# Performance work log

Hardware: AMD Instinct MI355X
Metric: run time of the kernel (lower is better)

Reference implementation:

```python
import jax, jax.numpy as jnp
import numpy as np

S, R = 512, 384            # N_seq, N_res
C_MSA, C_Z = 64, 128
C_HID, H = 32, 8
INF = 1e8
EPS = 1e-5


def _layernorm(x, w, b):
    mu = jnp.mean(x, axis=-1, keepdims=True)
    var = jnp.var(x, axis=-1, keepdims=True)
    return (x - mu) * jax.lax.rsqrt(var + EPS) * w + b


def setup_inputs() -> dict:
    key = jax.random.key(0)
    ks = jax.random.split(key, 8)
    d = {
        "m": jax.random.normal(ks[0], (S, R, C_MSA), dtype=jnp.float32),
        "z": jax.random.normal(ks[1], (R, R, C_Z), dtype=jnp.float32),
        "msa_mask": jnp.ones((S, R), dtype=jnp.float32),
        "z_mask": jnp.ones((R, R), dtype=jnp.float32),
        # learned parameters
        "ln_m_w": jnp.ones((C_MSA,), jnp.float32),
        "ln_m_b": jnp.zeros((C_MSA,), jnp.float32),
        "ln_z_w": jnp.ones((C_Z,), jnp.float32),
        "ln_z_b": jnp.zeros((C_Z,), jnp.float32),
        "w_v": jax.random.normal(ks[2], (C_MSA, H * C_HID), jnp.float32) * (1.0 / np.sqrt(C_MSA)),
        "w_g": jax.random.normal(ks[3], (C_MSA, H * C_HID), jnp.float32) * 0.02,
        "w_b": jax.random.normal(ks[4], (C_Z, H), jnp.float32) * (1.0 / np.sqrt(C_Z)),
        "w_o": jax.random.normal(ks[5], (H * C_HID, C_MSA), jnp.float32) * 0.02,
    }
    return d


def reference(m, z, msa_mask, z_mask, ln_m_w, ln_m_b, ln_z_w, ln_z_b, w_v, w_g, w_b, w_o):
    # m: [S, R, C_MSA], z: [R, R, C_Z]
    m_ln = _layernorm(m, ln_m_w, ln_m_b)
    v = (m_ln @ w_v).reshape(S, R, H, C_HID)                    # [S,R,H,C]
    g = jax.nn.sigmoid(m_ln @ w_g).reshape(S, R, H, C_HID)      # gating [S,R,H,C]
    b = _layernorm(z, ln_z_w, ln_z_b) @ w_b                     # pair bias [R,R,H]
    b = b + INF * (z_mask[..., None] - 1.0)                     # mask invalid pairs
    v = v * msa_mask[..., None, None]                           # mask MSA values
    w = jax.nn.softmax(b, axis=-2)                              # softmax over j (keys)
    # o[s,i,h,c] = sum_j w[i,j,h] * v[s,j,h,c]  (pair-weighted averaging)
    o = g * jnp.einsum('ijh,sjhd->sihd', w, v)                  # [S,R,H,C]
    out = o.reshape(S, R, H * C_HID) @ w_o                      # [S,R,C_MSA]
    return out
```

## Files before the change

### kernel.cpp

```cpp
#include <hip/hip_runtime.h>
#include <hip/hip_bf16.h>
#include <stdint.h>

#define S_DIM 512
#define R_DIM 384
#define CMSA 64
#define CZ 128
#define HH 8
#define CHID 32
#define HC 256
#define INF_V 1e8f
#define EPS_V 1e-5f

typedef __bf16 bf16x8 __attribute__((ext_vector_type(8)));
typedef float f32x4 __attribute__((ext_vector_type(4)));

__device__ __forceinline__ unsigned short f2bf(float f) {
  __hip_bfloat16 h = __float2bfloat16(f);
  return *reinterpret_cast<unsigned short*>(&h);
}
__device__ __forceinline__ float bf2f(unsigned short u) {
  __hip_bfloat16 h;
  *reinterpret_cast<unsigned short*>(&h) = u;
  return __bfloat162float(h);
}
__device__ __forceinline__ int4 pack8(const unsigned short* u) {
  int4 p;
  p.x = (int)u[0] | ((int)u[1] << 16);
  p.y = (int)u[2] | ((int)u[3] << 16);
  p.z = (int)u[4] | ((int)u[5] << 16);
  p.w = (int)u[6] | ((int)u[7] << 16);
  return p;
}

__device__ __forceinline__ float reduce8x(float* s, int cs7) {
  float t[4];
#pragma unroll
  for (int k = 0; k < 4; ++k) {
    float snd = (cs7 & 1) ? s[2 * k] : s[2 * k + 1];
    float rcv = __shfl_xor(snd, 1);
    t[k] = ((cs7 & 1) ? s[2 * k + 1] : s[2 * k]) + rcv;
  }
  float r[2];
#pragma unroll
  for (int k = 0; k < 2; ++k) {
    float snd = (cs7 & 2) ? t[2 * k] : t[2 * k + 1];
    float rcv = __shfl_xor(snd, 2);
    r[k] = ((cs7 & 2) ? t[2 * k + 1] : t[2 * k]) + rcv;
  }
  float snd = (cs7 & 4) ? r[0] : r[1];
  float rcv = __shfl_xor(snd, 4);
  return ((cs7 & 4) ? r[1] : r[0]) + rcv;
}

__global__ __launch_bounds__(256) void k_bias(
    const float* __restrict__ z, const float* __restrict__ z_mask,
    const float* __restrict__ lnw, const float* __restrict__ lnb,
    const float* __restrict__ w_b, float* __restrict__ b_out) {
  int tid = threadIdx.x, lane = tid & 63, wv = tid >> 6;
  int cs = lane & 15, ps = lane >> 4;
  int cs7 = cs & 7;

  float4 wba[2][4], wbb[2][4], lnw4[2];
  float aU[8] = {0, 0, 0, 0, 0, 0, 0, 0};
  float aA[8] = {0, 0, 0, 0, 0, 0, 0, 0};
#pragma unroll
  for (int q = 0; q < 2; ++q) {
    int c0 = q * 64 + cs * 4;
    lnw4[q] = *reinterpret_cast<const float4*>(&lnw[c0]);
    float4 lnb4 = *reinterpret_cast<const float4*>(&lnb[c0]);
#pragma unroll
    for (int e = 0; e < 4; ++e) {
      wba[q][e] = *reinterpret_cast<const float4*>(&w_b[(size_t)(c0 + e) * HH]);
      wbb[q][e] = *reinterpret_cast<const float4*>(&w_b[(size_t)(c0 + e) * HH + 4]);
      float lw = reinterpret_cast<const float*>(&lnw4[q])[e];
      float lb = reinterpret_cast<const float*>(&lnb4)[e];
      aU[0] += lw * wba[q][e].x; aU[1] += lw * wba[q][e].y;
      aU[2] += lw * wba[q][e].z; aU[3] += lw * wba[q][e].w;
      aU[4] += lw * wbb[q][e].x; aU[5] += lw * wbb[q][e].y;
      aU[6] += lw * wbb[q][e].z; aU[7] += lw * wbb[q][e].w;
      aA[0] += lb * wba[q][e].x; aA[1] += lb * wba[q][e].y;
      aA[2] += lb * wba[q][e].z; aA[3] += lb * wba[q][e].w;
      aA[4] += lb * wbb[q][e].x; aA[5] += lb * wbb[q][e].y;
      aA[6] += lb * wbb[q][e].z; aA[7] += lb * wbb[q][e].w;
    }
  }
#pragma unroll
  for (int h = 0; h < 8; ++h) {
    aU[h] += __shfl_xor(aU[h], 8);
    aA[h] += __shfl_xor(aA[h], 8);
  }
  float U_l = reduce8x(aU, cs7);
  float A_l = reduce8x(aA, cs7);

  const int NTASK = (R_DIM * R_DIM) / 4;
  for (int task = blockIdx.x * 4 + wv; task < NTASK; task += gridDim.x * 4) {
    int g = task * 4 + ps;
    const float* zp = z + (size_t)g * CZ;
    float4 zv[2];
    zv[0] = *reinterpret_cast<const float4*>(zp + cs * 4);
    zv[1] = *reinterpret_cast<const float4*>(zp + 64 + cs * 4);
    float sz = 0.f, sz2 = 0.f;
    float s[8] = {0, 0, 0, 0, 0, 0, 0, 0};
#pragma unroll
    for (int q = 0; q < 2; ++q)
#pragma unroll
      for (int e = 0; e < 4; ++e) {
        float x = reinterpret_cast<const float*>(&zv[q])[e];
        float lw = reinterpret_cast<const float*>(&lnw4[q])[e];
        sz += x; sz2 += x * x;
        float zn = x * lw;
        s[0] += zn * wba[q][e].x; s[1] += zn * wba[q][e].y;
        s[2] += zn * wba[q][e].z; s[3] += zn * wba[q][e].w;
        s[4] += zn * wbb[q][e].x; s[5] += zn * wbb[q][e].y;
        s[6] += zn * wbb[q][e].z; s[7] += zn * wbb[q][e].w;
      }
#pragma unroll
    for (int d = 1; d <= 8; d <<= 1) {
      sz += __shfl_xor(sz, d);
      sz2 += __shfl_xor(sz2, d);
    }
#pragma unroll
    for (int h = 0; h < 8; ++h) s[h] += __shfl_xor(s[h], 8);
    float S = reduce8x(s, cs7);
    float mu = sz * (1.f / CZ);
    float var = sz2 * (1.f / CZ) - mu * mu;
    float rs = rsqrtf(var + EPS_V);
    float b = rs * S + A_l - rs * mu * U_l + INF_V * (z_mask[g] - 1.f);
    if (cs < 8) {
      int i = g / R_DIM, j = g - i * R_DIM;
      b_out[((size_t)i * HH + cs) * R_DIM + j] = b;
    }
  }
}

__global__ __launch_bounds__(128) void k_softmax(
    const float* __restrict__ b_in, unsigned short* __restrict__ w_bf) {
  int row = blockIdx.x;
  int i = row / HH, h = row - i * HH;
  const float* bp = b_in + (size_t)row * R_DIM;
  int t = threadIdx.x;
  float v[3];
  float mx = -INFINITY;
#pragma unroll
  for (int k = 0; k < 3; ++k) { v[k] = bp[t + 128 * k]; mx = fmaxf(mx, v[k]); }
  __shared__ float red[128];
  red[t] = mx; __syncthreads();
  for (int off = 64; off > 0; off >>= 1) {
    if (t < off) red[t] = fmaxf(red[t], red[t + off]);
    __syncthreads();
  }
  mx = red[0]; __syncthreads();
  float sum = 0.f;
#pragma unroll
  for (int k = 0; k < 3; ++k) { v[k] = __expf(v[k] - mx); sum += v[k]; }
  red[t] = sum; __syncthreads();
  for (int off = 64; off > 0; off >>= 1) {
    if (t < off) red[t] += red[t + off];
    __syncthreads();
  }
  float inv = 1.0f / red[0];
  unsigned short* wp = w_bf + ((size_t)h * R_DIM + i) * R_DIM;
#pragma unroll
  for (int k = 0; k < 3; ++k) wp[t + 128 * k] = f2bf(v[k] * inv);
}

__global__ __launch_bounds__(512) void k_vg(
    const float* __restrict__ m, const float* __restrict__ msa_mask,
    const float* __restrict__ lnw, const float* __restrict__ lnb,
    const float* __restrict__ w_v, const float* __restrict__ w_g,
    unsigned short* __restrict__ Vt, unsigned short* __restrict__ g_ws) {
  extern __shared__ char lds[];
  const int A_OFF = 0;
  const int WV_OFF = 16384;
  const int WG_OFF = 49152;
  const int T_OFF = 81920;
  const int M_OFF = 151552;
  int tid = threadIdx.x, l = tid & 63, wv = tid >> 6;
  int b = blockIdx.x;
  int s = b / 3;
  int res0 = (b % 3) * 128;
  size_t row0 = (size_t)s * R_DIM + res0;

  if (tid < 128) *reinterpret_cast<float*>(&lds[M_OFF + tid * 4]) = msa_mask[row0 + tid];

  for (int it = 0; it < 4; ++it) {
    int G = it * 512 + tid;
    int hcr = G >> 3, slot = G & 7;
    unsigned short uv[8], ug[8];
#pragma unroll
    for (int e = 0; e < 8; ++e) {
      uv[e] = f2bf(w_v[(size_t)(slot * 8 + e) * HC + hcr]);
      ug[e] = f2bf(w_g[(size_t)(slot * 8 + e) * HC + hcr]);
    }
    int swz = hcr * 128 + ((slot ^ (hcr & 7)) << 4);
    *reinterpret_cast<int4*>(&lds[WV_OFF + swz]) = pack8(uv);
    *reinterpret_cast<int4*>(&lds[WG_OFF + swz]) = pack8(ug);
  }

  float lw = lnw[l], lbv = lnb[l];
  for (int q = 0; q < 16; ++q) {
    int r = wv * 16 + q;
    float x = m[(row0 + r) * CMSA + l];
    float sm = x, s2 = x * x;
#pragma unroll
    for (int d = 1; d < 64; d <<= 1) { sm += __shfl_xor(sm, d); s2 += __shfl_xor(s2, d); }
    float mu = sm * (1.f / 64.f);
    float var = s2 * (1.f / 64.f) - mu * mu;
    float nv = (x - mu) * rsqrtf(var + EPS_V) * lw + lbv;
    *reinterpret_cast<unsigned short*>(
        &lds[A_OFF + r * 128 + (((l >> 3) ^ (r & 7)) << 4) + (l & 7) * 2]) = f2bf(nv);
  }
  __syncthreads();

  f32x4 zz = {0.f, 0.f, 0.f, 0.f};
  f32x4 vacc[2][8];
#pragma unroll
  for (int a = 0; a < 2; ++a)
#pragma unroll
    for (int n = 0; n < 8; ++n) vacc[a][n] = zz;
#pragma unroll
  for (int kc = 0; kc < 2; ++kc) {
    bf16x8 af[2], bfv[8];
#pragma unroll
    for (int mf = 0; mf < 2; ++mf) {
      int row = ((wv & 3) * 2 + mf) * 16 + (l & 15);
      af[mf] = *reinterpret_cast<const bf16x8*>(
          &lds[A_OFF + row * 128 + (((kc * 4 + (l >> 4)) ^ (row & 7)) << 4)]);
    }
#pragma unroll
    for (int nf = 0; nf < 8; ++nf) {
      int row = ((wv >> 2) * 8 + nf) * 16 + (l & 15);
      bfv[nf] = *reinterpret_cast<const bf16x8*>(
          &lds[WV_OFF + row * 128 + (((kc * 4 + (l >> 4)) ^ (row & 7)) << 4)]);
    }
#pragma unroll
    for (int mf = 0; mf < 2; ++mf)
#pragma unroll
      for (int nf = 0; nf < 8; ++nf)
        vacc[mf][nf] = __builtin_amdgcn_mfma_f32_16x16x32_bf16(af[mf], bfv[nf], vacc[mf][nf], 0, 0, 0);
  }
#pragma unroll
  for (int mf = 0; mf < 2; ++mf) {
    int resb = ((wv & 3) * 2 + mf) * 16 + (l >> 4) * 4;
    float4 mk = *reinterpret_cast<const float4*>(&lds[M_OFF + resb * 4]);
#pragma unroll
    for (int nf = 0; nf < 8; ++nf) {
      int hc = ((wv >> 2) * 8 + nf) * 16 + (l & 15);
      ushort4 o;
      o.x = f2bf(vacc[mf][nf][0] * mk.x);
      o.y = f2bf(vacc[mf][nf][1] * mk.y);
      o.z = f2bf(vacc[mf][nf][2] * mk.z);
      o.w = f2bf(vacc[mf][nf][3] * mk.w);
      *reinterpret_cast<ushort4*>(&lds[T_OFF + hc * 272 + resb * 2]) = o;
    }
  }
  __syncthreads();
  for (int it = 0; it < 8; ++it) {
    int G = it * 512 + tid;
    int hc = G >> 4, gi = G & 15;
    int4 d = *reinterpret_cast<const int4*>(&lds[T_OFF + hc * 272 + gi * 16]);
    *reinterpret_cast<int4*>(&Vt[((size_t)s * HC + hc) * R_DIM + res0 + gi * 8]) = d;
  }

  f32x4 gacc[2][8];
#pragma unroll
  for (int a = 0; a < 2; ++a)
#pragma unroll
    for (int n = 0; n < 8; ++n) gacc[a][n] = zz;
#pragma unroll
  for (int kc = 0; kc < 2; ++kc) {
    bf16x8 af[2], bfg[8];
#pragma unroll
    for (int mf = 0; mf < 2; ++mf) {
      int row = ((wv & 3) * 2 + mf) * 16 + (l & 15);
      af[mf] = *reinterpret_cast<const bf16x8*>(
          &lds[A_OFF + row * 128 + (((kc * 4 + (l >> 4)) ^ (row & 7)) << 4)]);
    }
#pragma unroll
    for (int nf = 0; nf < 8; ++nf) {
      int row = ((wv >> 2) * 8 + nf) * 16 + (l & 15);
      bfg[nf] = *reinterpret_cast<const bf16x8*>(
          &lds[WG_OFF + row * 128 + (((kc * 4 + (l >> 4)) ^ (row & 7)) << 4)]);
    }
#pragma unroll
    for (int mf = 0; mf < 2; ++mf)
#pragma unroll
      for (int nf = 0; nf < 8; ++nf)
        gacc[mf][nf] = __builtin_amdgcn_mfma_f32_16x16x32_bf16(af[mf], bfg[nf], gacc[mf][nf], 0, 0, 0);
  }
#pragma unroll
  for (int mf = 0; mf < 2; ++mf)
#pragma unroll
    for (int nf = 0; nf < 8; ++nf) {
      int hc = ((wv >> 2) * 8 + nf) * 16 + (l & 15);
#pragma unroll
      for (int reg = 0; reg < 4; ++reg) {
        int res = ((wv & 3) * 2 + mf) * 16 + (l >> 4) * 4 + reg;
        float sg = 1.f / (1.f + __expf(-gacc[mf][nf][reg]));
        g_ws[(row0 + res) * HC + hc] = f2bf(sg);
      }
    }
}

__global__ __launch_bounds__(512) void k_wavg(
    const unsigned short* __restrict__ Vt, const unsigned short* __restrict__ g_ws,
    const unsigned short* __restrict__ w_bf, const float* __restrict__ w_o,
    float* __restrict__ out) {
  extern __shared__ char lds[];
  const int A_OFF = 0;
  const int B_OFF = 32768;
  const int P_OFF = 45056;
  const int W_OFF = 94208;
  int tid = threadIdx.x, l = tid & 63, wv = tid >> 6;
  int bs = blockIdx.x >> 2, bi = blockIdx.x & 3;
  int s0 = bs * 8, i0 = bi * 96;

  for (int it = 0; it < 4; ++it) {
    int G = it * 512 + tid;
    int lrow = G >> 5, slot = G & 31;
    unsigned short u[8];
#pragma unroll
    for (int e = 0; e < 8; ++e) u[e] = f2bf(w_o[(size_t)(slot * 8 + e) * CMSA + lrow]);
    *reinterpret_cast<int4*>(&lds[W_OFF + lrow * 512 + ((slot ^ (lrow & 7)) << 4)]) = pack8(u);
  }

  int slotg = tid & 3;
  int rA0 = tid >> 2, rA1 = 128 + (tid >> 2);
  size_t vtb0 = ((size_t)(s0 + (rA0 >> 5)) * HC + (rA0 & 31)) * R_DIM + slotg * 8;
  size_t vtb1 = ((size_t)(s0 + (rA1 >> 5)) * HC + (rA1 & 31)) * R_DIM + slotg * 8;
  int ldsA0 = rA0 * 64 + ((slotg ^ (rA0 & 3)) << 4);
  int ldsA1 = rA1 * 64 + ((slotg ^ (rA1 & 3)) << 4);
  int rB = tid >> 2;
  size_t wbase = (size_t)(i0 + rB) * R_DIM + slotg * 8;
  int ldsB = rB * 64 + ((slotg ^ (rB & 3)) << 4);

  int aoff[4], boff[3], poff[6];
#pragma unroll
  for (int mf = 0; mf < 4; ++mf) {
    int row = ((wv & 3) * 4 + mf) * 16 + (l & 15);
    aoff[mf] = row * 64 + (((l >> 4) ^ (row & 3)) << 4);
  }
#pragma unroll
  for (int nf = 0; nf < 3; ++nf) {
    int row = ((wv >> 2) * 3 + nf) * 16 + (l & 15);
    boff[nf] = row * 64 + (((l >> 4) ^ (row & 3)) << 4);
  }
#pragma unroll
  for (int mf = 0; mf < 6; ++mf) {
    int row = (wv * 6 + mf) * 16 + (l & 15);
    poff[mf] = row * 64 + (((l >> 4) ^ (row & 3)) << 4);
  }

  f32x4 zz = {0.f, 0.f, 0.f, 0.f};
  f32x4 pacc[6][4];
#pragma unroll
  for (int a = 0; a < 6; ++a)
#pragma unroll
    for (int n = 0; n < 4; ++n) pacc[a][n] = zz;

  for (int h = 0; h < 8; ++h) {
    const unsigned short* VtA = Vt + (size_t)h * 32 * R_DIM;
    const unsigned short* WB = w_bf + (size_t)h * R_DIM * R_DIM;
    f32x4 acc[4][3];
#pragma unroll
    for (int a = 0; a < 4; ++a)
#pragma unroll
      for (int n = 0; n < 3; ++n) acc[a][n] = zz;

    {
      int4 va0 = *reinterpret_cast<const int4*>(VtA + vtb0);
      int4 va1 = *reinterpret_cast<const int4*>(VtA + vtb1);
      int4 vb;
      if (tid < 384) vb = *reinterpret_cast<const int4*>(WB + wbase);
      *reinterpret_cast<int4*>(&lds[A_OFF + ldsA0]) = va0;
      *reinterpret_cast<int4*>(&lds[A_OFF + ldsA1]) = va1;
      if (tid < 384) *reinterpret_cast<int4*>(&lds[B_OFF + ldsB]) = vb;
    }
    __syncthreads();

    for (int t = 0; t < 12; ++t) {
      int cur = t & 1;
      int4 va0, va1, vb;
      if (t < 11) {
        int j0n = (t + 1) * 32;
        va0 = *reinterpret_cast<const int4*>(VtA + vtb0 + j0n);
        va1 = *reinterpret_cast<const int4*>(VtA + vtb1 + j0n);
        if (tid < 384) vb = *reinterpret_cast<const int4*>(WB + wbase + j0n);
      }
      const char* ab = &lds[A_OFF + cur * 16384];
      const char* bb = &lds[B_OFF + cur * 6144];
      bf16x8 af[4], bfr[3];
#pragma unroll
      for (int mf = 0; mf < 4; ++mf) af[mf] = *reinterpret_cast<const bf16x8*>(ab + aoff[mf]);
#pragma unroll
      for (int nf = 0; nf < 3; ++nf) bfr[nf] = *reinterpret_cast<const bf16x8*>(bb + boff[nf]);
#pragma unroll
      for (int mf = 0; mf < 4; ++mf)
#pragma unroll
        for (int nf = 0; nf < 3; ++nf)
          acc[mf][nf] = __builtin_amdgcn_mfma_f32_16x16x32_bf16(af[mf], bfr[nf], acc[mf][nf], 0, 0, 0);
      if (t < 11) {
        int nxt = cur ^ 1;
        *reinterpret_cast<int4*>(&lds[A_OFF + nxt * 16384 + ldsA0]) = va0;
        *reinterpret_cast<int4*>(&lds[A_OFF + nxt * 16384 + ldsA1]) = va1;
        if (tid < 384) *reinterpret_cast<int4*>(&lds[B_OFF + nxt * 6144 + ldsB]) = vb;
      }
      __syncthreads();
    }

#pragma unroll
    for (int mf = 0; mf < 4; ++mf) {
      int MT = (wv & 3) * 4 + mf;
      int sl = MT >> 1;
      int c0 = (MT & 1) * 16 + (l >> 4) * 4;
#pragma unroll
      for (int nf = 0; nf < 3; ++nf) {
        int il = ((wv >> 2) * 3 + nf) * 16 + (l & 15);
        size_t gidx = ((size_t)(s0 + sl) * R_DIM + i0 + il) * HC + h * 32 + c0;
        ushort4 g4 = *reinterpret_cast<const ushort4*>(g_ws + gidx);
        int prow = sl * 96 + il;
        ushort4 og;
        og.x = f2bf(acc[mf][nf][0] * bf2f(g4.x));
        og.y = f2bf(acc[mf][nf][1] * bf2f(g4.y));
        og.z = f2bf(acc[mf][nf][2] * bf2f(g4.z));
        og.w = f2bf(acc[mf][nf][3] * bf2f(g4.w));
        *reinterpret_cast<ushort4*>(
            &lds[P_OFF + prow * 64 + (((c0 >> 3) ^ (prow & 3)) << 4) + (c0 & 7) * 2]) = og;
      }
    }
    __syncthreads();

    {
      bf16x8 pa[6], bw[4];
#pragma unroll
      for (int nt = 0; nt < 4; ++nt) {
        int lrow = nt * 16 + (l & 15);
        bw[nt] = *reinterpret_cast<const bf16x8*>(
            &lds[W_OFF + lrow * 512 + (((h * 4 + (l >> 4)) ^ (lrow & 7)) << 4)]);
      }
#pragma unroll
      for (int mf = 0; mf < 6; ++mf) pa[mf] = *reinterpret_cast<const bf16x8*>(&lds[P_OFF + poff[mf]]);
#pragma unroll
      for (int mf = 0; mf < 6; ++mf)
#pragma unroll
        for (int nt = 0; nt < 4; ++nt)
          pacc[mf][nt] = __builtin_amdgcn_mfma_f32_16x16x32_bf16(pa[mf], bw[nt], pacc[mf][nt], 0, 0, 0);
    }
    __syncthreads();
  }

#pragma unroll
  for (int mf = 0; mf < 6; ++mf) {
#pragma unroll
    for (int reg = 0; reg < 4; ++reg) {
      int prow = (wv * 6 + mf) * 16 + (l >> 4) * 4 + reg;
      int sl = prow / 96;
      int il = prow - sl * 96;
      size_t orow = (size_t)(s0 + sl) * R_DIM + i0 + il;
#pragma unroll
      for (int nt = 0; nt < 4; ++nt)
        out[orow * CMSA + nt * 16 + (l & 15)] = pacc[mf][nt][reg];
    }
  }
}

extern "C" void kernel_launch(void* const* d_in, const int* in_sizes, int n_in,
                              void* d_out, int out_size, void* d_ws, size_t ws_size,
                              hipStream_t stream) {
  (void)in_sizes; (void)n_in; (void)out_size; (void)ws_size;
  const float* m        = (const float*)d_in[0];
  const float* z        = (const float*)d_in[1];
  const float* msa_mask = (const float*)d_in[2];
  const float* z_mask   = (const float*)d_in[3];
  const float* ln_m_w   = (const float*)d_in[4];
  const float* ln_m_b   = (const float*)d_in[5];
  const float* ln_z_w   = (const float*)d_in[6];
  const float* ln_z_b   = (const float*)d_in[7];
  const float* w_v      = (const float*)d_in[8];
  const float* w_g      = (const float*)d_in[9];
  const float* w_b      = (const float*)d_in[10];
  const float* w_o      = (const float*)d_in[11];
  float* out = (float*)d_out;

  char* ws = (char*)d_ws;
  unsigned short* Vt   = (unsigned short*)ws;
  unsigned short* g_ws = (unsigned short*)(ws + 100663296ull);
  float*          b_ws = (float*)(ws + 201326592ull);
  unsigned short* w_bf = (unsigned short*)(ws + 206045184ull);

  k_bias<<<dim3(2304), dim3(256), 0, stream>>>(
      z, z_mask, ln_z_w, ln_z_b, w_b, b_ws);
  k_softmax<<<dim3(R_DIM * HH), dim3(128), 0, stream>>>(b_ws, w_bf);
  k_vg<<<dim3(S_DIM * R_DIM / 128), dim3(512), 152064, stream>>>(
      m, msa_mask, ln_m_w, ln_m_b, w_v, w_g, Vt, g_ws);
  k_wavg<<<dim3(256), dim3(512), 126976, stream>>>(Vt, g_ws, w_bf, w_o, out);
}
```

Before: 398.6 us.

## Precompute bf16 weight images and shrink k_vg LDS to raise occupancy

Adds a small prep kernel that converts w_v, w_g and w_o to swizzled bf16 images once per call, so k_vg and k_wavg copy them with vector loads instead of every block re-converting strided fp32 weights. k_vg drops its transpose staging buffer and reuses one weight region for V and then G, cutting LDS from about 148KB to about 48KB so several blocks can share a CU. The V GEMM is transposed (weights as the A operand) so results can be written straight to Vt without LDS staging. LayerNorm now loads float4 vectors with a 4-lane reduction. This adds a kernel launch and an extra barrier plus weight reload, and the direct Vt stores are narrow 2-byte writes. The weight images sit in the b_ws region, which k_softmax has already consumed by then.

Result: faster. 347.0 us (-13.0%).

```diff
diff --git a/kernel.cpp b/kernel.cpp
--- a/kernel.cpp
+++ b/kernel.cpp
@@ -165,17 +165,38 @@
   for (int k = 0; k < 3; ++k) wp[t + 128 * k] = f2bf(v[k] * inv);
 }
 
-__global__ __launch_bounds__(512) void k_vg(
+__global__ __launch_bounds__(256) void k_prep(
+    const float* __restrict__ w_v, const float* __restrict__ w_g,
+    const float* __restrict__ w_o, unsigned short* __restrict__ wv_img,
+    unsigned short* __restrict__ wg_img, unsigned short* __restrict__ wo_img) {
+  int gid = blockIdx.x * 256 + threadIdx.x;
+  int mtx = gid >> 11, idx = gid & 2047;
+  unsigned short u[8];
+  if (mtx < 2) {
+    const float* w = mtx ? w_g : w_v;
+    unsigned short* img = mtx ? wg_img : wv_img;
+    int hcr = idx >> 3, slot = idx & 7;
+#pragma unroll
+    for (int e = 0; e < 8; ++e) u[e] = f2bf(w[(size_t)(slot * 8 + e) * HC + hcr]);
+    *reinterpret_cast<int4*>(&img[hcr * 64 + ((slot ^ (hcr & 7)) << 3)]) = pack8(u);
+  } else {
+    int lrow = idx >> 5, slot = idx & 31;
+#pragma unroll
+    for (int e = 0; e < 8; ++e) u[e] = f2bf(w_o[(size_t)(slot * 8 + e) * CMSA + lrow]);
+    *reinterpret_cast<int4*>(&wo_img[lrow * 256 + ((slot ^ (lrow & 7)) << 3)]) = pack8(u);
+  }
+}
+
+__global__ __launch_bounds__(512, 4) void k_vg(
     const float* __restrict__ m, const float* __restrict__ msa_mask,
     const float* __restrict__ lnw, const float* __restrict__ lnb,
-    const float* __restrict__ w_v, const float* __restrict__ w_g,
+    const unsigned short* __restrict__ wv_img,
+    const unsigned short* __restrict__ wg_img,
     unsigned short* __restrict__ Vt, unsigned short* __restrict__ g_ws) {
   extern __shared__ char lds[];
   const int A_OFF = 0;
-  const int WV_OFF = 16384;
-  const int WG_OFF = 49152;
-  const int T_OFF = 81920;
-  const int M_OFF = 151552;
+  const int W_OFF = 16384;
+  const int M_OFF = 49152;
   int tid = threadIdx.x, l = tid & 63, wv = tid >> 6;
   int b = blockIdx.x;
   int s = b / 3;
@@ -184,128 +205,153 @@
 
   if (tid < 128) *reinterpret_cast<float*>(&lds[M_OFF + tid * 4]) = msa_mask[row0 + tid];
 
-  for (int it = 0; it < 4; ++it) {
-    int G = it * 512 + tid;
-    int hcr = G >> 3, slot = G & 7;
-    unsigned short uv[8], ug[8];
-#pragma unroll
-    for (int e = 0; e < 8; ++e) {
-      uv[e] = f2bf(w_v[(size_t)(slot * 8 + e) * HC + hcr]);
-      ug[e] = f2bf(w_g[(size_t)(slot * 8 + e) * HC + hcr]);
-    }
-    int swz = hcr * 128 + ((slot ^ (hcr & 7)) << 4);
-    *reinterpret_cast<int4*>(&lds[WV_OFF + swz]) = pack8(uv);
-    *reinterpret_cast<int4*>(&lds[WG_OFF + swz]) = pack8(ug);
-  }
-
-  float lw = lnw[l], lbv = lnb[l];
-  for (int q = 0; q < 16; ++q) {
-    int r = wv * 16 + q;
-    float x = m[(row0 + r) * CMSA + l];
-    float sm = x, s2 = x * x;
-#pragma unroll
-    for (int d = 1; d < 64; d <<= 1) { sm += __shfl_xor(sm, d); s2 += __shfl_xor(s2, d); }
+  {
+    const int4* src = reinterpret_cast<const int4*>(wv_img);
+    int4* dst = reinterpret_cast<int4*>(&lds[W_OFF]);
+#pragma unroll
+    for (int p = 0; p < 4; ++p) dst[p * 512 + tid] = src[p * 512 + tid];
+  }
+
+  {
+    int row = tid >> 2, q = tid & 3;
+    const float* mp = m + (row0 + row) * CMSA + q * 16;
+    float4 x0 = *reinterpret_cast<const float4*>(mp);
+    float4 x1 = *reinterpret_cast<const float4*>(mp + 4);
+    float4 x2 = *reinterpret_cast<const float4*>(mp + 8);
+    float4 x3 = *reinterpret_cast<const float4*>(mp + 12);
+    float xs[16] = {x0.x, x0.y, x0.z, x0.w, x1.x, x1.y, x1.z, x1.w,
+                    x2.x, x2.y, x2.z, x2.w, x3.x, x3.y, x3.z, x3.w};
+    float sm = 0.f, s2 = 0.f;
+#pragma unroll
+    for (int e = 0; e < 16; ++e) { sm += xs[e]; s2 += xs[e] * xs[e]; }
+    sm += __shfl_xor(sm, 1); s2 += __shfl_xor(s2, 1);
+    sm += __shfl_xor(sm, 2); s2 += __shfl_xor(s2, 2);
     float mu = sm * (1.f / 64.f);
     float var = s2 * (1.f / 64.f) - mu * mu;
-    float nv = (x - mu) * rsqrtf(var + EPS_V) * lw + lbv;
-    *reinterpret_cast<unsigned short*>(
-        &lds[A_OFF + r * 128 + (((l >> 3) ^ (r & 7)) << 4) + (l & 7) * 2]) = f2bf(nv);
+    float rs = rsqrtf(var + EPS_V);
+    const float* lwp = lnw + q * 16;
+    const float* lbp = lnb + q * 16;
+    unsigned short u[16];
+#pragma unroll
+    for (int e = 0; e < 16; ++e)
+      u[e] = f2bf((xs[e] - mu) * rs * lwp[e] + lbp[e]);
+    int base = A_OFF + row * 128;
+    *reinterpret_cast<int4*>(&lds[base + (((2 * q) ^ (row & 7)) << 4)]) = pack8(u);
+    *reinterpret_cast<int4*>(&lds[base + (((2 * q + 1) ^ (row & 7)) << 4)]) = pack8(u + 8);
   }
   __syncthreads();
 
   f32x4 zz = {0.f, 0.f, 0.f, 0.f};
-  f32x4 vacc[2][8];
-#pragma unroll
-  for (int a = 0; a < 2; ++a)
-#pragma unroll
-    for (int n = 0; n < 8; ++n) vacc[a][n] = zz;
-#pragma unroll
-  for (int kc = 0; kc < 2; ++kc) {
-    bf16x8 af[2], bfv[8];
-#pragma unroll
-    for (int mf = 0; mf < 2; ++mf) {
-      int row = ((wv & 3) * 2 + mf) * 16 + (l & 15);
-      af[mf] = *reinterpret_cast<const bf16x8*>(
-          &lds[A_OFF + row * 128 + (((kc * 4 + (l >> 4)) ^ (row & 7)) << 4)]);
-    }
-#pragma unroll
-    for (int nf = 0; nf < 8; ++nf) {
-      int row = ((wv >> 2) * 8 + nf) * 16 + (l & 15);
-      bfv[nf] = *reinterpret_cast<const bf16x8*>(
-          &lds[WV_OFF + row * 128 + (((kc * 4 + (l >> 4)) ^ (row & 7)) << 4)]);
-    }
-#pragma unroll
-    for (int mf = 0; mf < 2; ++mf)
-#pragma unroll
-      for (int nf = 0; nf < 8; ++nf)
-        vacc[mf][nf] = __builtin_amdgcn_mfma_f32_16x16x32_bf16(af[mf], bfv[nf], vacc[mf][nf], 0, 0, 0);
-  }
-#pragma unroll
-  for (int mf = 0; mf < 2; ++mf) {
-    int resb = ((wv & 3) * 2 + mf) * 16 + (l >> 4) * 4;
-    float4 mk = *reinterpret_cast<const float4*>(&lds[M_OFF + resb * 4]);
-#pragma unroll
-    for (int nf = 0; nf < 8; ++nf) {
-      int hc = ((wv >> 2) * 8 + nf) * 16 + (l & 15);
-      ushort4 o;
-      o.x = f2bf(vacc[mf][nf][0] * mk.x);
-      o.y = f2bf(vacc[mf][nf][1] * mk.y);
-      o.z = f2bf(vacc[mf][nf][2] * mk.z);
-      o.w = f2bf(vacc[mf][nf][3] * mk.w);
-      *reinterpret_cast<ushort4*>(&lds[T_OFF + hc * 272 + resb * 2]) = o;
-    }
+
+  {
+    f32x4 vacc[2][8];
+#pragma unroll
+    for (int a = 0; a < 2; ++a)
+#pragma unroll
+      for (int n = 0; n < 8; ++n) vacc[a][n] = zz;
+#pragma unroll
+    for (int kc = 0; kc < 2; ++kc) {
+      bf16x8 aw[2];
+#pragma unroll
+      for (int mfa = 0; mfa < 2; ++mfa) {
+        int row = wv * 32 + mfa * 16 + (l & 15);
+        aw[mfa] = *reinterpret_cast<const bf16x8*>(
+            &lds[W_OFF + row * 128 + (((kc * 4 + (l >> 4)) ^ (row & 7)) << 4)]);
+      }
+#pragma unroll
+      for (int nh = 0; nh < 2; ++nh) {
+        bf16x8 bl[4];
+#pragma unroll
+        for (int nf = 0; nf < 4; ++nf) {
+          int res = (nh * 4 + nf) * 16 + (l & 15);
+          bl[nf] = *reinterpret_cast<const bf16x8*>(
+              &lds[A_OFF + res * 128 + (((kc * 4 + (l >> 4)) ^ (res & 7)) << 4)]);
+        }
+#pragma unroll
+        for (int mfa = 0; mfa < 2; ++mfa)
+#pragma unroll
+          for (int nf = 0; nf < 4; ++nf)
+            vacc[mfa][nh * 4 + nf] =
+                __builtin_amdgcn_mfma_f32_16x16x32_bf16(aw[mfa], bl[nf], vacc[mfa][nh * 4 + nf], 0, 0, 0);
+      }
+    }
+    float mk[8];
+#pragma unroll
+    for (int nf = 0; nf < 8; ++nf)
+      mk[nf] = *reinterpret_cast<const float*>(&lds[M_OFF + (nf * 16 + (l & 15)) * 4]);
+#pragma unroll
+    for (int mfa = 0; mfa < 2; ++mfa)
+#pragma unroll
+      for (int nf = 0; nf < 8; ++nf) {
+#pragma unroll
+        for (int reg = 0; reg < 4; ++reg) {
+          int hc = wv * 32 + mfa * 16 + (l >> 4) * 4 + reg;
+          Vt[((size_t)s * HC + hc) * R_DIM + res0 + nf * 16 + (l & 15)] =
+              f2bf(vacc[mfa][nf][reg] * mk[nf]);
+        }
+      }
   }
   __syncthreads();
-  for (int it = 0; it < 8; ++it) {
-    int G = it * 512 + tid;
-    int hc = G >> 4, gi = G & 15;
-    int4 d = *reinterpret_cast<const int4*>(&lds[T_OFF + hc * 272 + gi * 16]);
-    *reinterpret_cast<int4*>(&Vt[((size_t)s * HC + hc) * R_DIM + res0 + gi * 8]) = d;
-  }
-
-  f32x4 gacc[2][8];
-#pragma unroll
-  for (int a = 0; a < 2; ++a)
-#pragma unroll
-    for (int n = 0; n < 8; ++n) gacc[a][n] = zz;
-#pragma unroll
-  for (int kc = 0; kc < 2; ++kc) {
-    bf16x8 af[2], bfg[8];
-#pragma unroll
-    for (int mf = 0; mf < 2; ++mf) {
-      int row = ((wv & 3) * 2 + mf) * 16 + (l & 15);
-      af[mf] = *reinterpret_cast<const bf16x8*>(
-          &lds[A_OFF + row * 128 + (((kc * 4 + (l >> 4)) ^ (row & 7)) << 4)]);
-    }
-#pragma unroll
-    for (int nf = 0; nf < 8; ++nf) {
-      int row = ((wv >> 2) * 8 + nf) * 16 + (l & 15);
-      bfg[nf] = *reinterpret_cast<const bf16x8*>(
-          &lds[WG_OFF + row * 128 + (((kc * 4 + (l >> 4)) ^ (row & 7)) << 4)]);
-    }
-#pragma unroll
-    for (int mf = 0; mf < 2; ++mf)
-#pragma unroll
-      for (int nf = 0; nf < 8; ++nf)
-        gacc[mf][nf] = __builtin_amdgcn_mfma_f32_16x16x32_bf16(af[mf], bfg[nf], gacc[mf][nf], 0, 0, 0);
-  }
-#pragma unroll
-  for (int mf = 0; mf < 2; ++mf)
-#pragma unroll
-    for (int nf = 0; nf < 8; ++nf) {
-      int hc = ((wv >> 2) * 8 + nf) * 16 + (l & 15);
-#pragma unroll
-      for (int reg = 0; reg < 4; ++reg) {
-        int res = ((wv & 3) * 2 + mf) * 16 + (l >> 4) * 4 + reg;
-        float sg = 1.f / (1.f + __expf(-gacc[mf][nf][reg]));
-        g_ws[(row0 + res) * HC + hc] = f2bf(sg);
-      }
-    }
+
+  {
+    const int4* src = reinterpret_cast<const int4*>(wg_img);
+    int4* dst = reinterpret_cast<int4*>(&lds[W_OFF]);
+#pragma unroll
+    for (int p = 0; p < 4; ++p) dst[p * 512 + tid] = src[p * 512 + tid];
+  }
+  __syncthreads();
+
+  {
+    int resb = (wv & 3) * 32, hcb = (wv >> 2) * 128;
+    f32x4 gacc[2][8];
+#pragma unroll
+    for (int a = 0; a < 2; ++a)
+#pragma unroll
+      for (int n = 0; n < 8; ++n) gacc[a][n] = zz;
+#pragma unroll
+    for (int kc = 0; kc < 2; ++kc) {
+      bf16x8 al[2];
+#pragma unroll
+      for (int mfa = 0; mfa < 2; ++mfa) {
+        int row = resb + mfa * 16 + (l & 15);
+        al[mfa] = *reinterpret_cast<const bf16x8*>(
+            &lds[A_OFF + row * 128 + (((kc * 4 + (l >> 4)) ^ (row & 7)) << 4)]);
+      }
+#pragma unroll
+      for (int nh = 0; nh < 2; ++nh) {
+        bf16x8 bw[4];
+#pragma unroll
+        for (int nf = 0; nf < 4; ++nf) {
+          int col = hcb + (nh * 4 + nf) * 16 + (l & 15);
+          bw[nf] = *reinterpret_cast<const bf16x8*>(
+              &lds[W_OFF + col * 128 + (((kc * 4 + (l >> 4)) ^ (col & 7)) << 4)]);
+        }
+#pragma unroll
+        for (int mfa = 0; mfa < 2; ++mfa)
+#pragma unroll
+          for (int nf = 0; nf < 4; ++nf)
+            gacc[mfa][nh * 4 + nf] =
+                __builtin_amdgcn_mfma_f32_16x16x32_bf16(al[mfa], bw[nf], gacc[mfa][nh * 4 + nf], 0, 0, 0);
+      }
+    }
+#pragma unroll
+    for (int mfa = 0; mfa < 2; ++mfa)
+#pragma unroll
+      for (int nf = 0; nf < 8; ++nf) {
+#pragma unroll
+        for (int reg = 0; reg < 4; ++reg) {
+          int res = resb + mfa * 16 + (l >> 4) * 4 + reg;
+          int hc = hcb + nf * 16 + (l & 15);
+          float sg = 1.f / (1.f + __expf(-gacc[mfa][nf][reg]));
+          g_ws[(row0 + res) * HC + hc] = f2bf(sg);
+        }
+      }
+  }
 }
 
 __global__ __launch_bounds__(512) void k_wavg(
     const unsigned short* __restrict__ Vt, const unsigned short* __restrict__ g_ws,
-    const unsigned short* __restrict__ w_bf, const float* __restrict__ w_o,
+    const unsigned short* __restrict__ w_bf, const unsigned short* __restrict__ wo_img,
     float* __restrict__ out) {
   extern __shared__ char lds[];
   const int A_OFF = 0;
@@ -316,13 +362,11 @@
   int bs = blockIdx.x >> 2, bi = blockIdx.x & 3;
   int s0 = bs * 8, i0 = bi * 96;
 
-  for (int it = 0; it < 4; ++it) {
-    int G = it * 512 + tid;
-    int lrow = G >> 5, slot = G & 31;
-    unsigned short u[8];
-#pragma unroll
-    for (int e = 0; e < 8; ++e) u[e] = f2bf(w_o[(size_t)(slot * 8 + e) * CMSA + lrow]);
-    *reinterpret_cast<int4*>(&lds[W_OFF + lrow * 512 + ((slot ^ (lrow & 7)) << 4)]) = pack8(u);
+  {
+    const int4* src = reinterpret_cast<const int4*>(wo_img);
+    int4* dst = reinterpret_cast<int4*>(&lds[W_OFF]);
+#pragma unroll
+    for (int p = 0; p < 4; ++p) dst[p * 512 + tid] = src[p * 512 + tid];
   }
 
   int slotg = tid & 3;
@@ -488,11 +532,16 @@
   unsigned short* g_ws = (unsigned short*)(ws + 100663296ull);
   float*          b_ws = (float*)(ws + 201326592ull);
   unsigned short* w_bf = (unsigned short*)(ws + 206045184ull);
+  unsigned short* wv_img = (unsigned short*)(ws + 201326592ull);
+  unsigned short* wg_img = (unsigned short*)(ws + 201326592ull + 32768ull);
+  unsigned short* wo_img = (unsigned short*)(ws + 201326592ull + 65536ull);
 
   k_bias<<<dim3(2304), dim3(256), 0, stream>>>(
       z, z_mask, ln_z_w, ln_z_b, w_b, b_ws);
   k_softmax<<<dim3(R_DIM * HH), dim3(128), 0, stream>>>(b_ws, w_bf);
-  k_vg<<<dim3(S_DIM * R_DIM / 128), dim3(512), 152064, stream>>>(
-      m, msa_mask, ln_m_w, ln_m_b, w_v, w_g, Vt, g_ws);
-  k_wavg<<<dim3(256), dim3(512), 126976, stream>>>(Vt, g_ws, w_bf, w_o, out);
-}
+  k_prep<<<dim3(24), dim3(256), 0, stream>>>(
+      w_v, w_g, w_o, wv_img, wg_img, wo_img);
+  k_vg<<<dim3(S_DIM * R_DIM / 128), dim3(512), 49664, stream>>>(
+      m, msa_mask, ln_m_w, ln_m_b, wv_img, wg_img, Vt, g_ws);
+  k_wavg<<<dim3(256), dim3(512), 126976, stream>>>(Vt, g_ws, w_bf, wo_img, out);
+}
```
